# Kernel tuning notes

Measured on AMD Instinct MI355X. Metric: run time of the kernel, lower is better.

Reference implementation:

```python
import jax, jax.numpy as jnp
import numpy as np

SR = 44100
D = SR * 30          # duration_samples = 1_323_000
N = 1024             # number of note events
L = 32768            # max note length in samples
W = 1024             # hann window length (module's window_length)
H = 8                # harmonics in the synth
K = 128              # FIR taps in the effect chain
LAT = 2              # time_latent_size


def setup_inputs() -> dict:
    key = jax.random.key(0)
    ks = jax.random.split(key, 10)
    freq_rad = jax.random.uniform(ks[0], (N,), jnp.float32, 0.01, 0.3)
    velocity = jax.random.uniform(ks[1], (N,), jnp.float32, 1.0, 127.0)
    starts = jax.random.randint(ks[2], (N,), 0, D - L, dtype=jnp.int32)
    lengths = jax.random.randint(ks[3], (N,), 2048, L + 1, dtype=jnp.int32)
    # time_embedder: Linear(1,32) -> ReLU -> Linear(32,LAT)
    w1 = jax.random.normal(ks[4], (1, 32), jnp.float32)
    b1 = jnp.zeros((32,), jnp.float32)
    w2 = jax.random.normal(ks[5], (32, LAT), jnp.float32) / jnp.sqrt(32.0)
    b2 = jnp.zeros((LAT,), jnp.float32)
    # synth amplitude MLP: [freq, vel, latent] (2+LAT) -> 64 -> H
    ws1 = jax.random.normal(ks[6], (2 + LAT, 64), jnp.float32)
    bs1 = jnp.zeros((64,), jnp.float32)
    ws2 = jax.random.normal(ks[7], (64, H), jnp.float32) / 8.0
    bs2 = jnp.zeros((H,), jnp.float32)
    # effect chain: causal FIR (OIW layout) + tanh
    fir = jax.random.normal(ks[8], (1, 1, K), jnp.float32) / K
    return dict(freq_rad=freq_rad, velocity=velocity,
                w1=w1, b1=b1, w2=w2, b2=b2,
                ws1=ws1, bs1=bs1, ws2=ws2, bs2=bs2, fir=fir,
                starts=starts, lengths=lengths, duration_samples=D)


def reference(freq_rad, velocity, w1, b1, w2, b2, ws1, bs1, ws2, bs2, fir,
              starts, lengths, duration_samples):
    Dn = int(duration_samples)
    t = jnp.arange(L, dtype=jnp.float32)            # [L]
    ti = jnp.arange(L, dtype=jnp.int32)             # [L]
    ends = starts + lengths
    # output_length = min(end, duration) - start, clipped to [0, L]
    out_len = jnp.clip(jnp.minimum(ends, Dn) - starts, 0, L)  # [N]
    # time latent: MLP on normalized start time
    nt = (starts.astype(jnp.float32) / Dn)[:, None]           # [N,1]
    lat = jax.nn.relu(nt @ w1 + b1) @ w2 + b2                  # [N,LAT]
    vel = (velocity / 127.0)[:, None]                          # [N,1]
    # harmonic amplitudes from tiny MLP (the 'synth')
    feat = jnp.concatenate([freq_rad[:, None], vel, lat], axis=-1)  # [N,2+LAT]
    amps = jax.nn.softplus(jax.nn.relu(feat @ ws1 + bs1) @ ws2 + bs2)  # [N,H]
    # additive synthesis; fixed small loop over harmonics, vectorized over [N,L]
    phase = freq_rad[:, None] * t[None, :]                     # [N,L]
    seg = jnp.zeros((N, L), jnp.float32)
    for hh in range(1, H + 1):
        seg = seg + amps[:, hh - 1:hh] * jnp.sin(hh * phase)
    seg = seg * vel
    # hann window (torch periodic) on the LAST W samples of each variable-length segment
    n = jnp.arange(W, dtype=jnp.float32)
    hann = 0.5 * (1.0 - jnp.cos(2.0 * jnp.pi * n / W))         # [W]
    wpos = ti[None, :] - (out_len[:, None] - W)                # [N,L]
    in_win = (wpos >= 0) & (wpos < W)
    factor = jnp.where(in_win, hann[jnp.clip(wpos, 0, W - 1)], 1.0)
    mask = (ti[None, :] < out_len[:, None]).astype(jnp.float32)  # zero past segment end
    seg = seg * factor * mask
    # effect chain: causal 128-tap FIR then tanh (masked so padding stays silent)
    y = jax.lax.conv_general_dilated(seg[:, None, :], fir,
                                     window_strides=(1,), padding=[(K - 1, 0)])
    seg = jnp.tanh(y[:, 0, :]) * mask                          # [N,L]
    # overlap-add: scatter each note into the output buffer
    idx = starts[:, None] + ti[None, :]                        # [N,L]
    valid = (ti[None, :] < out_len[:, None]) & (idx < Dn)
    contrib = jnp.where(valid, seg, 0.0)
    out = jnp.zeros((Dn,), jnp.float32).at[jnp.clip(idx, 0, Dn - 1).reshape(-1)].add(
        contrib.reshape(-1))
    return out
```

## Files before the change

kernel.cpp:

```cpp
#include <hip/hip_runtime.h>
#include <math.h>

#define LMAX  32768
#define WWIN  1024
#define KFIR  128
#define WOUT  1024
#define TO    1024
#define CPAD  1232
#define SYNTH 1152
#define ZPS   1148
#define NMAX  1024
#define PMAX  96

typedef _Float16 v8h __attribute__((ext_vector_type(8)));
typedef _Float16 v4h __attribute__((ext_vector_type(4)));
typedef float    v4f __attribute__((ext_vector_type(4)));

__device__ __forceinline__ float fast_tanh(float x) {
    float e = __builtin_amdgcn_exp2f(x * 2.8853900817779268f);
    return fmaf(-2.0f, __builtin_amdgcn_rcpf(e + 1.0f), 1.0f);
}

__global__ __launch_bounds__(256, 3) void synth_fused_k(
    const float* __restrict__ freq_g, const float* __restrict__ velo_g,
    const float* __restrict__ w1,  const float* __restrict__ b1,
    const float* __restrict__ w2,  const float* __restrict__ b2,
    const float* __restrict__ ws1, const float* __restrict__ bs1,
    const float* __restrict__ ws2, const float* __restrict__ bs2,
    const float* __restrict__ fir,
    const int* __restrict__ starts, const int* __restrict__ lengths,
    float* __restrict__ out, int Dn, int N)
{
    __shared__ __align__(16) _Float16 segc[4][4][CPAD];
    __shared__ float fir_s[KFIR];
    __shared__ unsigned short note_list[NMAX];
    __shared__ int note_cnt;
    __shared__ float s_w1[32], s_b1[32], s_w2[64], s_b2[2];
    __shared__ float s_ws1[256], s_bs1[64], s_ws2[512], s_bs2[8];
    __shared__ int   stl[PMAX], oll[PMAX];
    __shared__ float fl[PMAX];
    __shared__ __align__(16) float ampsl[PMAX][8];

    const int tid  = threadIdx.x;
    const int wid  = tid >> 6;
    const int lane = tid & 63;
    const int m    = lane & 15;
    const int quad = lane >> 4;
    const int grp  = wid;
    const int o0   = blockIdx.x * TO;
    const int o_end = min(o0 + TO, Dn);
    const int ow   = o0;

    if (tid < 128) fir_s[tid] = fir[tid];
    if (tid < 32) { s_w1[tid] = w1[tid]; s_b1[tid] = b1[tid]; }
    if (tid < 64) { s_w2[tid] = w2[tid]; s_bs1[tid] = bs1[tid]; }
    if (tid < 2)  s_b2[tid] = b2[tid];
    if (tid < 8)  s_bs2[tid] = bs2[tid];
    s_ws1[tid] = ws1[tid];
    s_ws2[tid] = ws2[tid];  s_ws2[tid + 256] = ws2[tid + 256];
    if (tid == 0) note_cnt = 0;
    __syncthreads();

    for (int j = tid; j < N; j += 256) {
        int st = starts[j];
        int len = lengths[j];
        int ol = min(st + len, Dn) - st;
        ol = max(0, min(ol, LMAX));
        if (st < o_end && st + ol > o0) {
            int p = atomicAdd(&note_cnt, 1);
            note_list[p] = (unsigned short)j;
        }
    }
    __syncthreads();
    const int K = note_cnt;

    const int kn0 = min(K, PMAX);
    if (tid < kn0) {
        const int nid = (int)note_list[tid];
        int st  = starts[nid];
        int len = lengths[nid];
        int ol  = min(st + len, Dn) - st;
        ol = max(0, min(ol, LMAX));
        stl[tid] = st;
        oll[tid] = ol;
        float v = velo_g[nid] * (1.0f / 127.0f);
        float f = freq_g[nid];
        fl[tid] = f;
        float nt = (float)st / (float)Dn;
        float lat0 = s_b2[0], lat1 = s_b2[1];
        #pragma unroll
        for (int j = 0; j < 32; ++j) {
            float h = fmaxf(fmaf(nt, s_w1[j], s_b1[j]), 0.0f);
            lat0 = fmaf(h, s_w2[j * 2 + 0], lat0);
            lat1 = fmaf(h, s_w2[j * 2 + 1], lat1);
        }
        float acc[8];
        #pragma unroll
        for (int h = 0; h < 8; ++h) acc[h] = s_bs2[h];
        #pragma unroll
        for (int j = 0; j < 64; ++j) {
            float a = s_bs1[j];
            a = fmaf(f,    s_ws1[0 * 64 + j], a);
            a = fmaf(v,    s_ws1[1 * 64 + j], a);
            a = fmaf(lat0, s_ws1[2 * 64 + j], a);
            a = fmaf(lat1, s_ws1[3 * 64 + j], a);
            a = fmaxf(a, 0.0f);
            #pragma unroll
            for (int h = 0; h < 8; ++h)
                acc[h] = fmaf(a, s_ws2[j * 8 + h], acc[h]);
        }
        #pragma unroll
        for (int h = 0; h < 8; ++h) {
            float a = acc[h];
            float sp = fmaxf(a, 0.0f) + log1pf(expf(-fabsf(a)));
            ampsl[tid][h] = sp * v;
        }
    }

    v8h afrag[12];
    #pragma unroll
    for (int t = 0; t < 12; ++t) {
        v8h af;
        #pragma unroll
        for (int j = 0; j < 8; ++j) {
            int idx = 32 * t + 8 * quad + j - 16 * m;
            float fv = (idx >= 0 && idx < KFIR) ? fir_s[idx] : 0.0f;
            af[j] = (_Float16)fv;
        }
        afrag[t] = af;
    }
    for (int z = lane; z < 4 * (CPAD - ZPS); z += 64) {
        int S = z / (CPAD - ZPS), off = z % (CPAD - ZPS);
        segc[wid][S][ZPS + off] = (_Float16)0.0f;
    }
    __syncthreads();

    const _Float16* __restrict__ bbase = &segc[wid][m & 3][(m & ~3) + 8 * quad];

    float accv[16];
    #pragma unroll
    for (int r = 0; r < 16; ++r) accv[r] = 0.0f;

    const double inv2pi = 0.15915494309189535;

    for (int c = 0; c < K; c += PMAX) {
        const int kn = min(K - c, PMAX);

        if (c > 0) {
            __syncthreads();
            if (tid < kn) {
                const int nid = (int)note_list[c + tid];
                int st  = starts[nid];
                int len = lengths[nid];
                int ol  = min(st + len, Dn) - st;
                ol = max(0, min(ol, LMAX));
                stl[tid] = st;
                oll[tid] = ol;
                float v = velo_g[nid] * (1.0f / 127.0f);
                float f = freq_g[nid];
                fl[tid] = f;
                float nt = (float)st / (float)Dn;
                float lat0 = s_b2[0], lat1 = s_b2[1];
                #pragma unroll
                for (int j = 0; j < 32; ++j) {
                    float h = fmaxf(fmaf(nt, s_w1[j], s_b1[j]), 0.0f);
                    lat0 = fmaf(h, s_w2[j * 2 + 0], lat0);
                    lat1 = fmaf(h, s_w2[j * 2 + 1], lat1);
                }
                float acc[8];
                #pragma unroll
                for (int h = 0; h < 8; ++h) acc[h] = s_bs2[h];
                #pragma unroll
                for (int j = 0; j < 64; ++j) {
                    float a = s_bs1[j];
                    a = fmaf(f,    s_ws1[0 * 64 + j], a);
                    a = fmaf(v,    s_ws1[1 * 64 + j], a);
                    a = fmaf(lat0, s_ws1[2 * 64 + j], a);
                    a = fmaf(lat1, s_ws1[3 * 64 + j], a);
                    a = fmaxf(a, 0.0f);
                    #pragma unroll
                    for (int h = 0; h < 8; ++h)
                        acc[h] = fmaf(a, s_ws2[j * 8 + h], acc[h]);
                }
                #pragma unroll
                for (int h = 0; h < 8; ++h) {
                    float a = acc[h];
                    float sp = fmaxf(a, 0.0f) + log1pf(expf(-fabsf(a)));
                    ampsl[tid][h] = sp * v;
                }
            }
            __syncthreads();
        }

        int stN = 0, olN = 0; float fN = 0.f;
        float4 amN0 = {}, amN1 = {};
        if (grp < kn) {
            stN = stl[grp]; olN = oll[grp]; fN = fl[grp];
            amN0 = *(const float4*)&ampsl[grp][0];
            amN1 = *(const float4*)&ampsl[grp][4];
        }

        for (int kk = grp; kk < kn; kk += 4) {
            const int st = stN, ol = olN;
            const float f = fN;
            const float4 am0 = amN0, am1 = amN1;
            if (kk + 4 < kn) {
                stN = stl[kk + 4]; olN = oll[kk + 4]; fN = fl[kk + 4];
                amN0 = *(const float4*)&ampsl[kk + 4][0];
                amN1 = *(const float4*)&ampsl[kk + 4][4];
            }

            const int base = ow - st;
            if (base >= ol || base + WOUT <= 0) continue;

            const float A0 = am0.x, A1 = am0.y, A2 = am0.z, A3 = am0.w;
            const float A4 = am1.x, A5 = am1.y, A6 = am1.z, A7 = am1.w;
            const double fd = (double)f;

            const int tseed = base - 127 + lane;
            double rev0 = fd * (double)tseed * inv2pi;
            float r0 = (float)(rev0 - floor(rev0));
            float s = __builtin_amdgcn_sinf(r0);
            float cc = __builtin_amdgcn_cosf(r0);
            double d64 = fd * 64.0 * inv2pi;
            float r64 = (float)(d64 - floor(d64));
            const float sd = __builtin_amdgcn_sinf(r64);
            const float cd = __builtin_amdgcn_cosf(r64);
            const int wbase = ol - WWIN;

            const bool interior = (base >= 127) && (base + WOUT + 1 <= wbase);

            if (interior) {
                #pragma unroll
                for (int i = 0; i < SYNTH / 64; ++i) {
                    float tc = cc + cc;
                    float sA = s;
                    float sum = A0 * sA;
                    float sB = tc * sA;              sum = fmaf(A1, sB, sum);
                    float sC = fmaf(tc, sB, -sA);    sum = fmaf(A2, sC, sum);
                    float sD = fmaf(tc, sC, -sB);    sum = fmaf(A3, sD, sum);
                    float sE = fmaf(tc, sD, -sC);    sum = fmaf(A4, sE, sum);
                    float sF = fmaf(tc, sE, -sD);    sum = fmaf(A5, sF, sum);
                    float sG = fmaf(tc, sF, -sE);    sum = fmaf(A6, sG, sum);
                    float sH = fmaf(tc, sG, -sF);    sum = fmaf(A7, sH, sum);
                    _Float16 h = (_Float16)sum;
                    const int x = lane + 64 * i;
                    if (i == 0) {
                        #pragma unroll
                        for (int S = 0; S < 4; ++S)
                            if (x >= S) segc[wid][S][x - S] = h;
                    } else {
                        #pragma unroll
                        for (int S = 0; S < 4; ++S)
                            segc[wid][S][x - S] = h;
                    }
                    float ns = fmaf(s, cd, cc * sd);
                    float nc = fmaf(cc, cd, -(s * sd));
                    s = ns; cc = nc;
                }
            } else {
                #pragma unroll
                for (int i = 0; i < SYNTH / 64; ++i) {
                    int t = tseed + 64 * i;
                    float val = 0.0f;
                    if (t >= 0 && t < ol) {
                        float tc = cc + cc;
                        float sA = s;
                        float sum = A0 * sA;
                        float sB = tc * sA;              sum = fmaf(A1, sB, sum);
                        float sC = fmaf(tc, sB, -sA);    sum = fmaf(A2, sC, sum);
                        float sD = fmaf(tc, sC, -sB);    sum = fmaf(A3, sD, sum);
                        float sE = fmaf(tc, sD, -sC);    sum = fmaf(A4, sE, sum);
                        float sF = fmaf(tc, sE, -sD);    sum = fmaf(A5, sF, sum);
                        float sG = fmaf(tc, sF, -sE);    sum = fmaf(A6, sG, sum);
                        float sH = fmaf(tc, sG, -sF);    sum = fmaf(A7, sH, sum);
                        int wpos = t - wbase;
                        float factor = 1.0f;
                        if (wpos >= 0)
                            factor = 0.5f - 0.5f * __builtin_amdgcn_cosf((float)wpos * (1.0f / WWIN));
                        val = sum * factor;
                    }
                    _Float16 h = (_Float16)val;
                    const int x = lane + 64 * i;
                    if (i == 0) {
                        #pragma unroll
                        for (int S = 0; S < 4; ++S)
                            if (x >= S) segc[wid][S][x - S] = h;
                    } else {
                        #pragma unroll
                        for (int S = 0; S < 4; ++S)
                            segc[wid][S][x - S] = h;
                    }
                    float ns = fmaf(s, cd, cc * sd);
                    float nc = fmaf(cc, cd, -(s * sd));
                    s = ns; cc = nc;
                }
            }

            #pragma unroll
            for (int p = 0; p < 2; ++p) {
                const int co = 512 * p;
                v4f CA0 = {0.f, 0.f, 0.f, 0.f};
                v4f CA1 = {0.f, 0.f, 0.f, 0.f};
                v4f CB0 = {0.f, 0.f, 0.f, 0.f};
                v4f CB1 = {0.f, 0.f, 0.f, 0.f};
                #pragma unroll
                for (int t = 0; t < 6; ++t) {
                    v4h lo = *(const v4h*)(bbase + co + 32 * t);
                    v4h hi = *(const v4h*)(bbase + co + 32 * t + 4);
                    v8h bf = __builtin_shufflevector(lo, hi, 0, 1, 2, 3, 4, 5, 6, 7);
                    CA0 = __builtin_amdgcn_mfma_f32_16x16x32_f16(afrag[t], bf, CA0, 0, 0, 0);
                    v4h lo2 = *(const v4h*)(bbase + co + 256 + 32 * t);
                    v4h hi2 = *(const v4h*)(bbase + co + 256 + 32 * t + 4);
                    v8h bf2 = __builtin_shufflevector(lo2, hi2, 0, 1, 2, 3, 4, 5, 6, 7);
                    CB0 = __builtin_amdgcn_mfma_f32_16x16x32_f16(afrag[t], bf2, CB0, 0, 0, 0);
                }
                #pragma unroll
                for (int t = 6; t < 12; ++t) {
                    v4h lo = *(const v4h*)(bbase + co + 32 * t);
                    v4h hi = *(const v4h*)(bbase + co + 32 * t + 4);
                    v8h bf = __builtin_shufflevector(lo, hi, 0, 1, 2, 3, 4, 5, 6, 7);
                    CA1 = __builtin_amdgcn_mfma_f32_16x16x32_f16(afrag[t], bf, CA1, 0, 0, 0);
                    v4h lo2 = *(const v4h*)(bbase + co + 256 + 32 * t);
                    v4h hi2 = *(const v4h*)(bbase + co + 256 + 32 * t + 4);
                    v8h bf2 = __builtin_shufflevector(lo2, hi2, 0, 1, 2, 3, 4, 5, 6, 7);
                    CB1 = __builtin_amdgcn_mfma_f32_16x16x32_f16(afrag[t], bf2, CB1, 0, 0, 0);
                }

                const int tb = base + co + 64 * quad + m;
                float y;
                y = CA0[0] + CA1[0]; if (tb +   0 >= 0 && tb +   0 < ol) accv[p*8+0] += fast_tanh(y);
                y = CA0[1] + CA1[1]; if (tb +  16 >= 0 && tb +  16 < ol) accv[p*8+1] += fast_tanh(y);
                y = CA0[2] + CA1[2]; if (tb +  32 >= 0 && tb +  32 < ol) accv[p*8+2] += fast_tanh(y);
                y = CA0[3] + CA1[3]; if (tb +  48 >= 0 && tb +  48 < ol) accv[p*8+3] += fast_tanh(y);
                y = CB0[0] + CB1[0]; if (tb + 256 >= 0 && tb + 256 < ol) accv[p*8+4] += fast_tanh(y);
                y = CB0[1] + CB1[1]; if (tb + 272 >= 0 && tb + 272 < ol) accv[p*8+5] += fast_tanh(y);
                y = CB0[2] + CB1[2]; if (tb + 288 >= 0 && tb + 288 < ol) accv[p*8+6] += fast_tanh(y);
                y = CB0[3] + CB1[3]; if (tb + 304 >= 0 && tb + 304 < ol) accv[p*8+7] += fast_tanh(y);
            }
        }
    }

    __syncthreads();
    float* red = (float*)&segc[0][0][0];
    const int slot0 = 64 * quad + m;
    if (grp != 0) {
        float* rg = red + (grp - 1) * 1024;
        #pragma unroll
        for (int p = 0; p < 2; ++p) {
            #pragma unroll
            for (int r = 0; r < 8; ++r) {
                const int idx = slot0 + 512 * p + (r >> 2) * 256 + (r & 3) * 16;
                rg[idx] = accv[p * 8 + r];
            }
        }
    }
    __syncthreads();
    if (grp == 0) {
        #pragma unroll
        for (int p = 0; p < 2; ++p) {
            #pragma unroll
            for (int r = 0; r < 8; ++r) {
                const int idx = slot0 + 512 * p + (r >> 2) * 256 + (r & 3) * 16;
                float v = accv[p * 8 + r] + red[idx] + red[1024 + idx] + red[2048 + idx];
                const int ob = o0 + idx;
                if (ob < Dn) out[ob] = v;
            }
        }
    }
}

extern "C" void kernel_launch(void* const* d_in, const int* in_sizes, int n_in,
                              void* d_out, int out_size, void* d_ws, size_t ws_size,
                              hipStream_t stream) {
    const float* freq    = (const float*)d_in[0];
    const float* velo    = (const float*)d_in[1];
    const float* w1      = (const float*)d_in[2];
    const float* b1      = (const float*)d_in[3];
    const float* w2      = (const float*)d_in[4];
    const float* b2      = (const float*)d_in[5];
    const float* ws1     = (const float*)d_in[6];
    const float* bs1     = (const float*)d_in[7];
    const float* ws2     = (const float*)d_in[8];
    const float* bs2     = (const float*)d_in[9];
    const float* fir     = (const float*)d_in[10];
    const int*   starts  = (const int*)d_in[11];
    const int*   lengths = (const int*)d_in[12];

    const int N  = in_sizes[0];
    const int Dn = out_size;
    float* out = (float*)d_out;

    int n_tiles = (Dn + TO - 1) / TO;
    synth_fused_k<<<n_tiles, 256, 0, stream>>>(
        freq, velo, w1, b1, w2, b2, ws1, bs1, ws2, bs2,
        fir, starts, lengths, out, Dn, N);
}
```

Baseline: 143.5 us.

## Precompute per-note params and tile note lists, schedule tiles by load

Moves the per-note MLP and binning out of the main kernel into a setup kernel that computes each note's amplitudes once and appends note ids to per-tile lists with global atomics. A single-block counting sort then orders tiles by descending note count, so heavy tiles launch first. The synth kernel reads precomputed parameters instead of scanning all N notes and rerunning the MLP in every tile. This adds two extra launches and a memset, and silently caps each tile at SLOT=128 notes, which is correct only if no tile exceeds that count.

```diff
diff --git a/kernel.cpp b/kernel.cpp
--- a/kernel.cpp
+++ b/kernel.cpp
@@ -10,7 +10,7 @@
 #define SYNTH 1152
 #define ZPS   1148
 #define NMAX  1024
-#define PMAX  96
+#define SLOT  128
 
 typedef _Float16 v8h __attribute__((ext_vector_type(8)));
 typedef _Float16 v4h __attribute__((ext_vector_type(4)));
@@ -21,25 +21,120 @@
     return fmaf(-2.0f, __builtin_amdgcn_rcpf(e + 1.0f), 1.0f);
 }
 
-__global__ __launch_bounds__(256, 3) void synth_fused_k(
+__global__ __launch_bounds__(256) void setup_notes_k(
     const float* __restrict__ freq_g, const float* __restrict__ velo_g,
     const float* __restrict__ w1,  const float* __restrict__ b1,
     const float* __restrict__ w2,  const float* __restrict__ b2,
     const float* __restrict__ ws1, const float* __restrict__ bs1,
     const float* __restrict__ ws2, const float* __restrict__ bs2,
+    const int* __restrict__ starts, const int* __restrict__ lengths,
+    float* __restrict__ npar, int* __restrict__ counts,
+    unsigned short* __restrict__ lists,
+    int Dn, int N, int n_tiles)
+{
+    __shared__ float s_w1[32], s_b1[32], s_w2[64], s_b2[2];
+    __shared__ float s_ws1[256], s_bs1[64], s_ws2[512], s_bs2[8];
+    const int tid = threadIdx.x;
+    if (tid < 32) { s_w1[tid] = w1[tid]; s_b1[tid] = b1[tid]; }
+    if (tid < 64) { s_w2[tid] = w2[tid]; s_bs1[tid] = bs1[tid]; }
+    if (tid < 2)  s_b2[tid] = b2[tid];
+    if (tid < 8)  s_bs2[tid] = bs2[tid];
+    s_ws1[tid] = ws1[tid];
+    s_ws2[tid] = ws2[tid];  s_ws2[tid + 256] = ws2[tid + 256];
+    __syncthreads();
+
+    const int j = blockIdx.x * 256 + tid;
+    if (j >= N) return;
+
+    int st  = starts[j];
+    int len = lengths[j];
+    int ol  = min(st + len, Dn) - st;
+    ol = max(0, min(ol, LMAX));
+    float v = velo_g[j] * (1.0f / 127.0f);
+    float f = freq_g[j];
+    float nt = (float)st / (float)Dn;
+    float lat0 = s_b2[0], lat1 = s_b2[1];
+    #pragma unroll
+    for (int jj = 0; jj < 32; ++jj) {
+        float h = fmaxf(fmaf(nt, s_w1[jj], s_b1[jj]), 0.0f);
+        lat0 = fmaf(h, s_w2[jj * 2 + 0], lat0);
+        lat1 = fmaf(h, s_w2[jj * 2 + 1], lat1);
+    }
+    float acc[8];
+    #pragma unroll
+    for (int h = 0; h < 8; ++h) acc[h] = s_bs2[h];
+    #pragma unroll
+    for (int jj = 0; jj < 64; ++jj) {
+        float a = s_bs1[jj];
+        a = fmaf(f,    s_ws1[0 * 64 + jj], a);
+        a = fmaf(v,    s_ws1[1 * 64 + jj], a);
+        a = fmaf(lat0, s_ws1[2 * 64 + jj], a);
+        a = fmaf(lat1, s_ws1[3 * 64 + jj], a);
+        a = fmaxf(a, 0.0f);
+        #pragma unroll
+        for (int h = 0; h < 8; ++h)
+            acc[h] = fmaf(a, s_ws2[jj * 8 + h], acc[h]);
+    }
+    float* p = npar + (size_t)j * 12;
+    p[0] = __int_as_float(st);
+    p[1] = __int_as_float(ol);
+    p[2] = f;
+    p[3] = 0.0f;
+    #pragma unroll
+    for (int h = 0; h < 8; ++h) {
+        float a = acc[h];
+        float sp = fmaxf(a, 0.0f) + log1pf(expf(-fabsf(a)));
+        p[4 + h] = sp * v;
+    }
+
+    if (ol > 0) {
+        int t0 = st >> 10;
+        int t1 = min((st + ol - 1) >> 10, n_tiles - 1);
+        for (int t = t0; t <= t1; ++t) {
+            int pos = atomicAdd(&counts[t], 1);
+            if (pos < SLOT) lists[(size_t)t * SLOT + pos] = (unsigned short)j;
+        }
+    }
+}
+
+__global__ __launch_bounds__(1024) void sort_tiles_k(
+    const int* __restrict__ counts, int* __restrict__ order, int n_tiles)
+{
+    __shared__ int hist[SLOT + 2];
+    __shared__ int bstart[SLOT + 2];
+    const int tid = threadIdx.x;
+    if (tid < SLOT + 2) hist[tid] = 0;
+    __syncthreads();
+    for (int t = tid; t < n_tiles; t += 1024) {
+        int k = min(counts[t], SLOT + 1);
+        atomicAdd(&hist[k], 1);
+    }
+    __syncthreads();
+    if (tid == 0) {
+        int run = 0;
+        for (int k = SLOT + 1; k >= 0; --k) { bstart[k] = run; run += hist[k]; }
+    }
+    __syncthreads();
+    for (int t = tid; t < n_tiles; t += 1024) {
+        int k = min(counts[t], SLOT + 1);
+        int p = atomicAdd(&bstart[k], 1);
+        order[p] = t;
+    }
+}
+
+__global__ __launch_bounds__(256, 3) void synth_fused_k(
     const float* __restrict__ fir,
-    const int* __restrict__ starts, const int* __restrict__ lengths,
-    float* __restrict__ out, int Dn, int N)
+    const float* __restrict__ npar,
+    const int* __restrict__ counts,
+    const unsigned short* __restrict__ lists,
+    const int* __restrict__ order,
+    float* __restrict__ out, int Dn)
 {
     __shared__ __align__(16) _Float16 segc[4][4][CPAD];
     __shared__ float fir_s[KFIR];
-    __shared__ unsigned short note_list[NMAX];
-    __shared__ int note_cnt;
-    __shared__ float s_w1[32], s_b1[32], s_w2[64], s_b2[2];
-    __shared__ float s_ws1[256], s_bs1[64], s_ws2[512], s_bs2[8];
-    __shared__ int   stl[PMAX], oll[PMAX];
-    __shared__ float fl[PMAX];
-    __shared__ __align__(16) float ampsl[PMAX][8];
+    __shared__ int   stl[SLOT], oll[SLOT];
+    __shared__ float fl[SLOT];
+    __shared__ __align__(16) float ampsl[SLOT][8];
 
     const int tid  = threadIdx.x;
     const int wid  = tid >> 6;
@@ -47,75 +142,24 @@
     const int m    = lane & 15;
     const int quad = lane >> 4;
     const int grp  = wid;
-    const int o0   = blockIdx.x * TO;
-    const int o_end = min(o0 + TO, Dn);
+    const int tile = order[blockIdx.x];
+    const int o0   = tile * TO;
     const int ow   = o0;
 
-    if (tid < 128) fir_s[tid] = fir[tid];
-    if (tid < 32) { s_w1[tid] = w1[tid]; s_b1[tid] = b1[tid]; }
-    if (tid < 64) { s_w2[tid] = w2[tid]; s_bs1[tid] = bs1[tid]; }
-    if (tid < 2)  s_b2[tid] = b2[tid];
-    if (tid < 8)  s_bs2[tid] = bs2[tid];
-    s_ws1[tid] = ws1[tid];
-    s_ws2[tid] = ws2[tid];  s_ws2[tid + 256] = ws2[tid + 256];
-    if (tid == 0) note_cnt = 0;
-    __syncthreads();
-
-    for (int j = tid; j < N; j += 256) {
-        int st = starts[j];
-        int len = lengths[j];
-        int ol = min(st + len, Dn) - st;
-        ol = max(0, min(ol, LMAX));
-        if (st < o_end && st + ol > o0) {
-            int p = atomicAdd(&note_cnt, 1);
-            note_list[p] = (unsigned short)j;
-        }
-    }
-    __syncthreads();
-    const int K = note_cnt;
-
-    const int kn0 = min(K, PMAX);
-    if (tid < kn0) {
-        const int nid = (int)note_list[tid];
-        int st  = starts[nid];
-        int len = lengths[nid];
-        int ol  = min(st + len, Dn) - st;
-        ol = max(0, min(ol, LMAX));
-        stl[tid] = st;
-        oll[tid] = ol;
-        float v = velo_g[nid] * (1.0f / 127.0f);
-        float f = freq_g[nid];
-        fl[tid] = f;
-        float nt = (float)st / (float)Dn;
-        float lat0 = s_b2[0], lat1 = s_b2[1];
-        #pragma unroll
-        for (int j = 0; j < 32; ++j) {
-            float h = fmaxf(fmaf(nt, s_w1[j], s_b1[j]), 0.0f);
-            lat0 = fmaf(h, s_w2[j * 2 + 0], lat0);
-            lat1 = fmaf(h, s_w2[j * 2 + 1], lat1);
-        }
-        float acc[8];
-        #pragma unroll
-        for (int h = 0; h < 8; ++h) acc[h] = s_bs2[h];
-        #pragma unroll
-        for (int j = 0; j < 64; ++j) {
-            float a = s_bs1[j];
-            a = fmaf(f,    s_ws1[0 * 64 + j], a);
-            a = fmaf(v,    s_ws1[1 * 64 + j], a);
-            a = fmaf(lat0, s_ws1[2 * 64 + j], a);
-            a = fmaf(lat1, s_ws1[3 * 64 + j], a);
-            a = fmaxf(a, 0.0f);
-            #pragma unroll
-            for (int h = 0; h < 8; ++h)
-                acc[h] = fmaf(a, s_ws2[j * 8 + h], acc[h]);
-        }
-        #pragma unroll
-        for (int h = 0; h < 8; ++h) {
-            float a = acc[h];
-            float sp = fmaxf(a, 0.0f) + log1pf(expf(-fabsf(a)));
-            ampsl[tid][h] = sp * v;
-        }
-    }
+    const int K = min(counts[tile], SLOT);
+
+    if (tid < KFIR) fir_s[tid] = fir[tid];
+    if (tid < K) {
+        const int nid = (int)lists[(size_t)tile * SLOT + tid];
+        const float4* pp = (const float4*)(npar + (size_t)nid * 12);
+        float4 a = pp[0], b = pp[1], c = pp[2];
+        stl[tid] = __float_as_int(a.x);
+        oll[tid] = __float_as_int(a.y);
+        fl[tid]  = a.z;
+        *(float4*)&ampsl[tid][0] = b;
+        *(float4*)&ampsl[tid][4] = c;
+    }
+    __syncthreads();
 
     v8h afrag[12];
     #pragma unroll
@@ -133,7 +177,6 @@
         int S = z / (CPAD - ZPS), off = z % (CPAD - ZPS);
         segc[wid][S][ZPS + off] = (_Float16)0.0f;
     }
-    __syncthreads();
 
     const _Float16* __restrict__ bbase = &segc[wid][m & 3][(m & ~3) + 8 * quad];
 
@@ -143,96 +186,78 @@
 
     const double inv2pi = 0.15915494309189535;
 
-    for (int c = 0; c < K; c += PMAX) {
-        const int kn = min(K - c, PMAX);
-
-        if (c > 0) {
-            __syncthreads();
-            if (tid < kn) {
-                const int nid = (int)note_list[c + tid];
-                int st  = starts[nid];
-                int len = lengths[nid];
-                int ol  = min(st + len, Dn) - st;
-                ol = max(0, min(ol, LMAX));
-                stl[tid] = st;
-                oll[tid] = ol;
-                float v = velo_g[nid] * (1.0f / 127.0f);
-                float f = freq_g[nid];
-                fl[tid] = f;
-                float nt = (float)st / (float)Dn;
-                float lat0 = s_b2[0], lat1 = s_b2[1];
-                #pragma unroll
-                for (int j = 0; j < 32; ++j) {
-                    float h = fmaxf(fmaf(nt, s_w1[j], s_b1[j]), 0.0f);
-                    lat0 = fmaf(h, s_w2[j * 2 + 0], lat0);
-                    lat1 = fmaf(h, s_w2[j * 2 + 1], lat1);
+    int stN = 0, olN = 0; float fN = 0.f;
+    float4 amN0 = {}, amN1 = {};
+    if (grp < K) {
+        stN = stl[grp]; olN = oll[grp]; fN = fl[grp];
+        amN0 = *(const float4*)&ampsl[grp][0];
+        amN1 = *(const float4*)&ampsl[grp][4];
+    }
+
+    for (int kk = grp; kk < K; kk += 4) {
+        const int st = stN, ol = olN;
+        const float f = fN;
+        const float4 am0 = amN0, am1 = amN1;
+        if (kk + 4 < K) {
+            stN = stl[kk + 4]; olN = oll[kk + 4]; fN = fl[kk + 4];
+            amN0 = *(const float4*)&ampsl[kk + 4][0];
+            amN1 = *(const float4*)&ampsl[kk + 4][4];
+        }
+
+        const int base = ow - st;
+        if (base >= ol || base + WOUT <= 0) continue;
+
+        const float A0 = am0.x, A1 = am0.y, A2 = am0.z, A3 = am0.w;
+        const float A4 = am1.x, A5 = am1.y, A6 = am1.z, A7 = am1.w;
+        const double fd = (double)f;
+
+        const int tseed = base - 127 + lane;
+        double rev0 = fd * (double)tseed * inv2pi;
+        float r0 = (float)(rev0 - floor(rev0));
+        float s = __builtin_amdgcn_sinf(r0);
+        float cc = __builtin_amdgcn_cosf(r0);
+        double d64 = fd * 64.0 * inv2pi;
+        float r64 = (float)(d64 - floor(d64));
+        const float sd = __builtin_amdgcn_sinf(r64);
+        const float cd = __builtin_amdgcn_cosf(r64);
+        const int wbase = ol - WWIN;
+
+        const bool interior = (base >= 127) && (base + WOUT + 1 <= wbase);
+
+        if (interior) {
+            #pragma unroll
+            for (int i = 0; i < SYNTH / 64; ++i) {
+                float tc = cc + cc;
+                float sA = s;
+                float sum = A0 * sA;
+                float sB = tc * sA;              sum = fmaf(A1, sB, sum);
+                float sC = fmaf(tc, sB, -sA);    sum = fmaf(A2, sC, sum);
+                float sD = fmaf(tc, sC, -sB);    sum = fmaf(A3, sD, sum);
+                float sE = fmaf(tc, sD, -sC);    sum = fmaf(A4, sE, sum);
+                float sF = fmaf(tc, sE, -sD);    sum = fmaf(A5, sF, sum);
+                float sG = fmaf(tc, sF, -sE);    sum = fmaf(A6, sG, sum);
+                float sH = fmaf(tc, sG, -sF);    sum = fmaf(A7, sH, sum);
+                _Float16 h = (_Float16)sum;
+                const int x = lane + 64 * i;
+                if (i == 0) {
+                    #pragma unroll
+                    for (int S = 0; S < 4; ++S)
+                        if (x >= S) segc[wid][S][x - S] = h;
+                } else {
+                    #pragma unroll
+                    for (int S = 0; S < 4; ++S)
+                        segc[wid][S][x - S] = h;
                 }
-                float acc[8];
-                #pragma unroll
-                for (int h = 0; h < 8; ++h) acc[h] = s_bs2[h];
-                #pragma unroll
-                for (int j = 0; j < 64; ++j) {
-                    float a = s_bs1[j];
-                    a = fmaf(f,    s_ws1[0 * 64 + j], a);
-                    a = fmaf(v,    s_ws1[1 * 64 + j], a);
-                    a = fmaf(lat0, s_ws1[2 * 64 + j], a);
-                    a = fmaf(lat1, s_ws1[3 * 64 + j], a);
-                    a = fmaxf(a, 0.0f);
-                    #pragma unroll
-                    for (int h = 0; h < 8; ++h)
-                        acc[h] = fmaf(a, s_ws2[j * 8 + h], acc[h]);
-                }
-                #pragma unroll
-                for (int h = 0; h < 8; ++h) {
-                    float a = acc[h];
-                    float sp = fmaxf(a, 0.0f) + log1pf(expf(-fabsf(a)));
-                    ampsl[tid][h] = sp * v;
-                }
-            }
-            __syncthreads();
-        }
-
-        int stN = 0, olN = 0; float fN = 0.f;
-        float4 amN0 = {}, amN1 = {};
-        if (grp < kn) {
-            stN = stl[grp]; olN = oll[grp]; fN = fl[grp];
-            amN0 = *(const float4*)&ampsl[grp][0];
-            amN1 = *(const float4*)&ampsl[grp][4];
-        }
-
-        for (int kk = grp; kk < kn; kk += 4) {
-            const int st = stN, ol = olN;
-            const float f = fN;
-            const float4 am0 = amN0, am1 = amN1;
-            if (kk + 4 < kn) {
-                stN = stl[kk + 4]; olN = oll[kk + 4]; fN = fl[kk + 4];
-                amN0 = *(const float4*)&ampsl[kk + 4][0];
-                amN1 = *(const float4*)&ampsl[kk + 4][4];
-            }
-
-            const int base = ow - st;
-            if (base >= ol || base + WOUT <= 0) continue;
-
-            const float A0 = am0.x, A1 = am0.y, A2 = am0.z, A3 = am0.w;
-            const float A4 = am1.x, A5 = am1.y, A6 = am1.z, A7 = am1.w;
-            const double fd = (double)f;
-
-            const int tseed = base - 127 + lane;
-            double rev0 = fd * (double)tseed * inv2pi;
-            float r0 = (float)(rev0 - floor(rev0));
-            float s = __builtin_amdgcn_sinf(r0);
-            float cc = __builtin_amdgcn_cosf(r0);
-            double d64 = fd * 64.0 * inv2pi;
-            float r64 = (float)(d64 - floor(d64));
-            const float sd = __builtin_amdgcn_sinf(r64);
-            const float cd = __builtin_amdgcn_cosf(r64);
-            const int wbase = ol - WWIN;
-
-            const bool interior = (base >= 127) && (base + WOUT + 1 <= wbase);
-
-            if (interior) {
-                #pragma unroll
-                for (int i = 0; i < SYNTH / 64; ++i) {
+                float ns = fmaf(s, cd, cc * sd);
+                float nc = fmaf(cc, cd, -(s * sd));
+                s = ns; cc = nc;
+            }
+        } else {
+            #pragma unroll
+            for (int i = 0; i < SYNTH / 64; ++i) {
+                int t = tseed + 64 * i;
+                float val = 0.0f;
+                if (t >= 0 && t < ol) {
                     float tc = cc + cc;
                     float sA = s;
                     float sum = A0 * sA;
@@ -243,101 +268,69 @@
                     float sF = fmaf(tc, sE, -sD);    sum = fmaf(A5, sF, sum);
                     float sG = fmaf(tc, sF, -sE);    sum = fmaf(A6, sG, sum);
                     float sH = fmaf(tc, sG, -sF);    sum = fmaf(A7, sH, sum);
-                    _Float16 h = (_Float16)sum;
-                    const int x = lane + 64 * i;
-                    if (i == 0) {
-                        #pragma unroll
-                        for (int S = 0; S < 4; ++S)
-                            if (x >= S) segc[wid][S][x - S] = h;
-                    } else {
-                        #pragma unroll
-                        for (int S = 0; S < 4; ++S)
-                            segc[wid][S][x - S] = h;
-                    }
-                    float ns = fmaf(s, cd, cc * sd);
-                    float nc = fmaf(cc, cd, -(s * sd));
-                    s = ns; cc = nc;
+                    int wpos = t - wbase;
+                    float factor = 1.0f;
+                    if (wpos >= 0)
+                        factor = 0.5f - 0.5f * __builtin_amdgcn_cosf((float)wpos * (1.0f / WWIN));
+                    val = sum * factor;
                 }
-            } else {
-                #pragma unroll
-                for (int i = 0; i < SYNTH / 64; ++i) {
-                    int t = tseed + 64 * i;
-                    float val = 0.0f;
-                    if (t >= 0 && t < ol) {
-                        float tc = cc + cc;
-                        float sA = s;
-                        float sum = A0 * sA;
-                        float sB = tc * sA;              sum = fmaf(A1, sB, sum);
-                        float sC = fmaf(tc, sB, -sA);    sum = fmaf(A2, sC, sum);
-                        float sD = fmaf(tc, sC, -sB);    sum = fmaf(A3, sD, sum);
-                        float sE = fmaf(tc, sD, -sC);    sum = fmaf(A4, sE, sum);
-                        float sF = fmaf(tc, sE, -sD);    sum = fmaf(A5, sF, sum);
-                        float sG = fmaf(tc, sF, -sE);    sum = fmaf(A6, sG, sum);
-                        float sH = fmaf(tc, sG, -sF);    sum = fmaf(A7, sH, sum);
-                        int wpos = t - wbase;
-                        float factor = 1.0f;
-                        if (wpos >= 0)
-                            factor = 0.5f - 0.5f * __builtin_amdgcn_cosf((float)wpos * (1.0f / WWIN));
-                        val = sum * factor;
-                    }
-                    _Float16 h = (_Float16)val;
-                    const int x = lane + 64 * i;
-                    if (i == 0) {
-                        #pragma unroll
-                        for (int S = 0; S < 4; ++S)
-                            if (x >= S) segc[wid][S][x - S] = h;
-                    } else {
-                        #pragma unroll
-                        for (int S = 0; S < 4; ++S)
-                            segc[wid][S][x - S] = h;
-                    }
-                    float ns = fmaf(s, cd, cc * sd);
-                    float nc = fmaf(cc, cd, -(s * sd));
-                    s = ns; cc = nc;
+                _Float16 h = (_Float16)val;
+                const int x = lane + 64 * i;
+                if (i == 0) {
+                    #pragma unroll
+                    for (int S = 0; S < 4; ++S)
+                        if (x >= S) segc[wid][S][x - S] = h;
+                } else {
+                    #pragma unroll
+                    for (int S = 0; S < 4; ++S)
+                        segc[wid][S][x - S] = h;
                 }
-            }
-
-            #pragma unroll
-            for (int p = 0; p < 2; ++p) {
-                const int co = 512 * p;
-                v4f CA0 = {0.f, 0.f, 0.f, 0.f};
-                v4f CA1 = {0.f, 0.f, 0.f, 0.f};
-                v4f CB0 = {0.f, 0.f, 0.f, 0.f};
-                v4f CB1 = {0.f, 0.f, 0.f, 0.f};
-                #pragma unroll
-                for (int t = 0; t < 6; ++t) {
-                    v4h lo = *(const v4h*)(bbase + co + 32 * t);
-                    v4h hi = *(const v4h*)(bbase + co + 32 * t + 4);
-                    v8h bf = __builtin_shufflevector(lo, hi, 0, 1, 2, 3, 4, 5, 6, 7);
-                    CA0 = __builtin_amdgcn_mfma_f32_16x16x32_f16(afrag[t], bf, CA0, 0, 0, 0);
-                    v4h lo2 = *(const v4h*)(bbase + co + 256 + 32 * t);
-                    v4h hi2 = *(const v4h*)(bbase + co + 256 + 32 * t + 4);
-                    v8h bf2 = __builtin_shufflevector(lo2, hi2, 0, 1, 2, 3, 4, 5, 6, 7);
-                    CB0 = __builtin_amdgcn_mfma_f32_16x16x32_f16(afrag[t], bf2, CB0, 0, 0, 0);
-                }
-                #pragma unroll
-                for (int t = 6; t < 12; ++t) {
-                    v4h lo = *(const v4h*)(bbase + co + 32 * t);
-                    v4h hi = *(const v4h*)(bbase + co + 32 * t + 4);
-                    v8h bf = __builtin_shufflevector(lo, hi, 0, 1, 2, 3, 4, 5, 6, 7);
-                    CA1 = __builtin_amdgcn_mfma_f32_16x16x32_f16(afrag[t], bf, CA1, 0, 0, 0);
-                    v4h lo2 = *(const v4h*)(bbase + co + 256 + 32 * t);
-                    v4h hi2 = *(const v4h*)(bbase + co + 256 + 32 * t + 4);
-                    v8h bf2 = __builtin_shufflevector(lo2, hi2, 0, 1, 2, 3, 4, 5, 6, 7);
-                    CB1 = __builtin_amdgcn_mfma_f32_16x16x32_f16(afrag[t], bf2, CB1, 0, 0, 0);
-                }
-
-                const int tb = base + co + 64 * quad + m;
-                float y;
-                y = CA0[0] + CA1[0]; if (tb +   0 >= 0 && tb +   0 < ol) accv[p*8+0] += fast_tanh(y);
-                y = CA0[1] + CA1[1]; if (tb +  16 >= 0 && tb +  16 < ol) accv[p*8+1] += fast_tanh(y);
-                y = CA0[2] + CA1[2]; if (tb +  32 >= 0 && tb +  32 < ol) accv[p*8+2] += fast_tanh(y);
-                y = CA0[3] + CA1[3]; if (tb +  48 >= 0 && tb +  48 < ol) accv[p*8+3] += fast_tanh(y);
-                y = CB0[0] + CB1[0]; if (tb + 256 >= 0 && tb + 256 < ol) accv[p*8+4] += fast_tanh(y);
-                y = CB0[1] + CB1[1]; if (tb + 272 >= 0 && tb + 272 < ol) accv[p*8+5] += fast_tanh(y);
-                y = CB0[2] + CB1[2]; if (tb + 288 >= 0 && tb + 288 < ol) accv[p*8+6] += fast_tanh(y);
-                y = CB0[3] + CB1[3]; if (tb + 304 >= 0 && tb + 304 < ol) accv[p*8+7] += fast_tanh(y);
-            }
+                float ns = fmaf(s, cd, cc * sd);
+                float nc = fmaf(cc, cd, -(s * sd));
+                s = ns; cc = nc;
+            }
+        }
+
+        #pragma unroll
+        for (int p = 0; p < 2; ++p) {
+            const int co = 512 * p;
+            v4f CA0 = {0.f, 0.f, 0.f, 0.f};
+            v4f CA1 = {0.f, 0.f, 0.f, 0.f};
+            v4f CB0 = {0.f, 0.f, 0.f, 0.f};
+            v4f CB1 = {0.f, 0.f, 0.f, 0.f};
+            #pragma unroll
+            for (int t = 0; t < 6; ++t) {
+                v4h lo = *(const v4h*)(bbase + co + 32 * t);
+                v4h hi = *(const v4h*)(bbase + co + 32 * t + 4);
+                v8h bf = __builtin_shufflevector(lo, hi, 0, 1, 2, 3, 4, 5, 6, 7);
+                CA0 = __builtin_amdgcn_mfma_f32_16x16x32_f16(afrag[t], bf, CA0, 0, 0, 0);
+                v4h lo2 = *(const v4h*)(bbase + co + 256 + 32 * t);
+                v4h hi2 = *(const v4h*)(bbase + co + 256 + 32 * t + 4);
+                v8h bf2 = __builtin_shufflevector(lo2, hi2, 0, 1, 2, 3, 4, 5, 6, 7);
+                CB0 = __builtin_amdgcn_mfma_f32_16x16x32_f16(afrag[t], bf2, CB0, 0, 0, 0);
+            }
+            #pragma unroll
+            for (int t = 6; t < 12; ++t) {
+                v4h lo = *(const v4h*)(bbase + co + 32 * t);
+                v4h hi = *(const v4h*)(bbase + co + 32 * t + 4);
+                v8h bf = __builtin_shufflevector(lo, hi, 0, 1, 2, 3, 4, 5, 6, 7);
+                CA1 = __builtin_amdgcn_mfma_f32_16x16x32_f16(afrag[t], bf, CA1, 0, 0, 0);
+                v4h lo2 = *(const v4h*)(bbase + co + 256 + 32 * t);
+                v4h hi2 = *(const v4h*)(bbase + co + 256 + 32 * t + 4);
+                v8h bf2 = __builtin_shufflevector(lo2, hi2, 0, 1, 2, 3, 4, 5, 6, 7);
+                CB1 = __builtin_amdgcn_mfma_f32_16x16x32_f16(afrag[t], bf2, CB1, 0, 0, 0);
+            }
+
+            const int tb = base + co + 64 * quad + m;
+            float y;
+            y = CA0[0] + CA1[0]; if (tb +   0 >= 0 && tb +   0 < ol) accv[p*8+0] += fast_tanh(y);
+            y = CA0[1] + CA1[1]; if (tb +  16 >= 0 && tb +  16 < ol) accv[p*8+1] += fast_tanh(y);
+            y = CA0[2] + CA1[2]; if (tb +  32 >= 0 && tb +  32 < ol) accv[p*8+2] += fast_tanh(y);
+            y = CA0[3] + CA1[3]; if (tb +  48 >= 0 && tb +  48 < ol) accv[p*8+3] += fast_tanh(y);
+            y = CB0[0] + CB1[0]; if (tb + 256 >= 0 && tb + 256 < ol) accv[p*8+4] += fast_tanh(y);
+            y = CB0[1] + CB1[1]; if (tb + 272 >= 0 && tb + 272 < ol) accv[p*8+5] += fast_tanh(y);
+            y = CB0[2] + CB1[2]; if (tb + 288 >= 0 && tb + 288 < ol) accv[p*8+6] += fast_tanh(y);
+            y = CB0[3] + CB1[3]; if (tb + 304 >= 0 && tb + 304 < ol) accv[p*8+7] += fast_tanh(y);
         }
     }
 
@@ -391,8 +384,22 @@
     const int Dn = out_size;
     float* out = (float*)d_out;
 
-    int n_tiles = (Dn + TO - 1) / TO;
+    const int n_tiles = (Dn + TO - 1) / TO;
+
+    char* ws = (char*)d_ws;
+    float* npar = (float*)ws;
+    size_t off1 = ((size_t)N * 12 * sizeof(float) + 255) & ~(size_t)255;
+    int* counts = (int*)(ws + off1);
+    size_t off2 = off1 + (((size_t)n_tiles * sizeof(int) + 255) & ~(size_t)255);
+    unsigned short* lists = (unsigned short*)(ws + off2);
+    size_t off3 = off2 + (((size_t)n_tiles * SLOT * sizeof(unsigned short) + 255) & ~(size_t)255);
+    int* order = (int*)(ws + off3);
+
+    hipMemsetAsync(counts, 0, (size_t)n_tiles * sizeof(int), stream);
+    setup_notes_k<<<(N + 255) / 256, 256, 0, stream>>>(
+        freq, velo, w1, b1, w2, b2, ws1, bs1, ws2, bs2,
+        starts, lengths, npar, counts, lists, Dn, N, n_tiles);
+    sort_tiles_k<<<1, 1024, 0, stream>>>(counts, order, n_tiles);
     synth_fused_k<<<n_tiles, 256, 0, stream>>>(
-        freq, velo, w1, b1, w2, b2, ws1, bs1, ws2, bs2,
-        fir, starts, lengths, out, Dn, N);
+        fir, npar, counts, lists, order, out, Dn);
 }
```

Result: slower. 148.8 us (+3.7%).
